# Performance work log

Hardware: AMD Instinct MI355X
Metric: run time of the kernel (lower is better)

## Reference

```python
import jax, jax.numpy as jnp
import numpy as np

LMAX = 3
D_IN = 16    # sum(2l+1) for l=0..3
D_OUT = 156  # sum over the 34 CG instructions of (2*l3+1)


def _build_sparse_cg():
    """Build the concatenated sparse CG index lists (mu1, mu2, mu3) and
    coefficients, mirroring TensorProduct.__init__: loop over all
    (l1, l2, l3) paths with l3 <= LMAX, take nonzeros of the real-basis
    Wigner-3j tensor (nonzero pattern: |m1' +- m2'| == |m3'|), offset the
    indices by the per-irrep block offsets, and concatenate.
    Coefficient values are deterministic synthetic stand-ins with the
    correct sparsity structure and component-normalization scale."""
    rs = np.random.RandomState(0)
    off_in = [0, 1, 4, 9]  # block offsets for l = 0..3 (block dim 2l+1)
    mu1, mu2, mu3, vals = [], [], [], []
    off3 = 0
    for l1 in range(LMAX + 1):
        for l2 in range(LMAX + 1):
            for l3 in range(abs(l1 - l2), min(l1 + l2, LMAX) + 1):
                for m1 in range(2 * l1 + 1):
                    for m2 in range(2 * l2 + 1):
                        a, b = m1 - l1, m2 - l2
                        for m3 in range(2 * l3 + 1):
                            c = m3 - l3
                            if abs(a + b) == abs(c) or abs(a - b) == abs(c):
                                mu1.append(off_in[l1] + m1)
                                mu2.append(off_in[l2] + m2)
                                mu3.append(off3 + m3)
                                vals.append(rs.randn() / np.sqrt(2 * l3 + 1))
                off3 += 2 * l3 + 1
    assert off3 == D_OUT
    return (np.asarray(mu1, np.int32), np.asarray(mu2, np.int32),
            np.asarray(mu3, np.int32), np.asarray(vals, np.float32))


def setup_inputs() -> dict:
    key = jax.random.key(0)
    k1, k2 = jax.random.split(key)
    B, C = 1024, 128
    x = jax.random.normal(k1, (B, D_IN, C), dtype=jnp.float32)
    y = jax.random.normal(k2, (B, D_IN, C), dtype=jnp.float32)
    mu1, mu2, mu3, cg = _build_sparse_cg()
    return {
        "x": x,
        "y": y,
        "cg": jnp.asarray(cg),
        "mu1": jnp.asarray(mu1),
        "mu2": jnp.asarray(mu2),
        "mu3": jnp.asarray(mu3),
    }


def reference(x, y, cg, mu1, mu2, mu3):
    # Fused equivalent of the per-batch / per-instruction Python loops:
    # out[b, mu3[k], c] += cg[k] * x[b, mu1[k], c] * y[b, mu2[k], c]
    terms = x[:, mu1, :] * cg[None, :, None] * y[:, mu2, :]  # [B, K, C]
    out = jnp.zeros((x.shape[0], D_OUT, x.shape[2]), dtype=x.dtype)
    return out.at[:, mu3, :].add(terms)
```

## Files before the change

### kernel.cpp

```cpp
#include <hip/hip_runtime.h>
#include <utility>


#define D_IN_ 16
#define D_OUT_ 156
#define C_ 128
#define KMAX_ 2048

struct CGRows {
    int n;
    int start[D_OUT_ + 1];
    int k[KMAX_];
    int m1[KMAX_];
    int m2[KMAX_];
};

constexpr CGRows build_rows() {
    int mu1[KMAX_] = {}, mu2[KMAX_] = {}, mu3[KMAX_] = {};
    int n = 0;
    const int off_in[4] = {0, 1, 4, 9};
    int off3 = 0;
    for (int l1 = 0; l1 <= 3; ++l1) {
        for (int l2 = 0; l2 <= 3; ++l2) {
            int lo = l1 > l2 ? l1 - l2 : l2 - l1;
            int hi = (l1 + l2) < 3 ? (l1 + l2) : 3;
            for (int l3 = lo; l3 <= hi; ++l3) {
                for (int m1 = 0; m1 < 2 * l1 + 1; ++m1) {
                    for (int m2 = 0; m2 < 2 * l2 + 1; ++m2) {
                        int a = m1 - l1, b = m2 - l2;
                        for (int m3 = 0; m3 < 2 * l3 + 1; ++m3) {
                            int c = m3 - l3;
                            int s = a + b; if (s < 0) s = -s;
                            int d = a - b; if (d < 0) d = -d;
                            int e = c < 0 ? -c : c;
                            if (s == e || d == e) {
                                mu1[n] = off_in[l1] + m1;
                                mu2[n] = off_in[l2] + m2;
                                mu3[n] = off3 + m3;
                                ++n;
                            }
                        }
                    }
                }
                off3 += 2 * l3 + 1;
            }
        }
    }
    CGRows r{};
    r.n = n;
    int cnt[D_OUT_] = {};
    for (int i = 0; i < n; ++i) cnt[mu3[i]]++;
    r.start[0] = 0;
    for (int j = 0; j < D_OUT_; ++j) r.start[j + 1] = r.start[j] + cnt[j];
    int pos[D_OUT_] = {};
    for (int j = 0; j < D_OUT_; ++j) pos[j] = r.start[j];
    for (int i = 0; i < n; ++i) {
        int j = mu3[i];
        int p = pos[j]++;
        r.k[p] = i;
        r.m1[p] = mu1[i];
        r.m2[p] = mu2[i];
    }
    return r;
}

constexpr CGRows CG = build_rows();
constexpr int K = CG.n;
static_assert(K <= KMAX_, "KMAX too small");

constexpr int find_split() {
    int j = 0;
    while (CG.start[j] < CG.n / 2) ++j;
    return j;
}
constexpr int RSPLIT = find_split();

constexpr unsigned need1(int j0, int j1) {
    unsigned m = 0;
    for (int p = CG.start[j0]; p < CG.start[j1]; ++p) m |= 1u << CG.m1[p];
    return m;
}
constexpr unsigned need2(int j0, int j1) {
    unsigned m = 0;
    for (int p = CG.start[j0]; p < CG.start[j1]; ++p) m |= 1u << CG.m2[p];
    return m;
}

__device__ __constant__ CGRows dCG = build_rows();

__global__ void gather_cg(const float* __restrict__ cg, float* __restrict__ cgs) {
    int i = blockIdx.x * 256 + threadIdx.x;
    if (i < K) cgs[i] = cg[dCG.k[i]];
}

template <unsigned M, int I>
__device__ __forceinline__ void load1(float2 (&v)[D_IN_], const float* __restrict__ base) {
    if constexpr ((M >> I) & 1u) v[I] = *(const float2*)(base + I * C_);
    else v[I] = make_float2(0.0f, 0.0f);
}

template <unsigned M, int... Is>
__device__ __forceinline__ void load_masked(float2 (&v)[D_IN_], const float* __restrict__ base,
                                            std::integer_sequence<int, Is...>) {
    (load1<M, Is>(v, base), ...);
}

template <int Base, int... Ts>
__device__ __forceinline__ float2 row_sum2(const float* __restrict__ cgs,
                                           const float2 (&xv)[D_IN_],
                                           const float2 (&yv)[D_IN_],
                                           std::integer_sequence<int, Ts...>) {
    float2 s = make_float2(0.0f, 0.0f);
    (((s.x = fmaf(cgs[Base + Ts], xv[CG.m1[Base + Ts]].x * yv[CG.m2[Base + Ts]].x, s.x)),
      (s.y = fmaf(cgs[Base + Ts], xv[CG.m1[Base + Ts]].y * yv[CG.m2[Base + Ts]].y, s.y))), ...);
    return s;
}

template <int J>
__device__ __forceinline__ void store_row(float* __restrict__ ob, const float* __restrict__ cgs,
                                          const float2 (&xv)[D_IN_], const float2 (&yv)[D_IN_]) {
    constexpr int base = CG.start[J];
    constexpr int nt = CG.start[J + 1] - CG.start[J];
    float2 s = row_sum2<base>(cgs, xv, yv, std::make_integer_sequence<int, nt>{});
    *(float2*)(ob + J * C_) = s;
}

template <int J0, int... Js>
__device__ __forceinline__ void rows_range(float* __restrict__ ob, const float* __restrict__ cgs,
                                           const float2 (&xv)[D_IN_], const float2 (&yv)[D_IN_],
                                           std::integer_sequence<int, Js...>) {
    (store_row<J0 + Js>(ob, cgs, xv, yv), ...);
}

__global__ __launch_bounds__(256, 2) void tp_cg_kernel(
    const float* __restrict__ x, const float* __restrict__ y,
    const float* __restrict__ cgs, float* __restrict__ out) {
    const int tid = (int)threadIdx.x;
    const int c2 = tid & 63;
    const int half = (tid >> 6) & 1;
    const int b = (int)((blockIdx.x << 1) | (tid >> 7));

    const float* xb = x + (size_t)b * (D_IN_ * C_) + c2 * 2;
    const float* yb = y + (size_t)b * (D_IN_ * C_) + c2 * 2;
    float* ob = out + (size_t)b * (D_OUT_ * C_) + c2 * 2;

    float2 xv[D_IN_], yv[D_IN_];
    if (half == 0) {
        constexpr unsigned m1 = need1(0, RSPLIT), m2 = need2(0, RSPLIT);
        load_masked<m1>(xv, xb, std::make_integer_sequence<int, D_IN_>{});
        load_masked<m2>(yv, yb, std::make_integer_sequence<int, D_IN_>{});
        rows_range<0>(ob, cgs, xv, yv, std::make_integer_sequence<int, RSPLIT>{});
    } else {
        constexpr unsigned m1 = need1(RSPLIT, D_OUT_), m2 = need2(RSPLIT, D_OUT_);
        load_masked<m1>(xv, xb, std::make_integer_sequence<int, D_IN_>{});
        load_masked<m2>(yv, yb, std::make_integer_sequence<int, D_IN_>{});
        rows_range<RSPLIT>(ob, cgs, xv, yv, std::make_integer_sequence<int, D_OUT_ - RSPLIT>{});
    }
}

extern "C" void kernel_launch(void* const* d_in, const int* in_sizes, int n_in,
                              void* d_out, int out_size, void* d_ws, size_t ws_size,
                              hipStream_t stream) {
    const float* x  = (const float*)d_in[0];
    const float* y  = (const float*)d_in[1];
    const float* cg = (const float*)d_in[2];
    float* out = (float*)d_out;
    float* cgs = (float*)d_ws;

    const int B = in_sizes[0] / (D_IN_ * C_);

    gather_cg<<<(K + 255) / 256, 256, 0, stream>>>(cg, cgs);

    const int nblocks = B / 2;
    tp_cg_kernel<<<nblocks, 256, 0, stream>>>(x, y, cgs, out);
}
```

Measured before the change: 109.5 us.

## Split output rows into quarters with one channel per thread

Work is now split four ways over the output rows instead of two, and each thread handles a single channel with scalar loads and stores instead of float2. The grid grows to four times as many blocks, and launch bounds are raised to ask for four blocks per SIMD-occupancy unit. The aim is more parallelism and less register pressure per thread, which should improve latency hiding. In exchange, input rows shared between quarters are loaded more than once, and the narrower 4-byte accesses give up the wider vector memory transactions.

```diff
diff --git a/kernel.cpp b/kernel.cpp
--- a/kernel.cpp
+++ b/kernel.cpp
@@ -68,12 +68,13 @@
 constexpr int K = CG.n;
 static_assert(K <= KMAX_, "KMAX too small");
 
-constexpr int find_split() {
+constexpr int findq(int i) {
+    int target = (CG.n * i) / 4;
     int j = 0;
-    while (CG.start[j] < CG.n / 2) ++j;
+    while (CG.start[j] < target) ++j;
     return j;
 }
-constexpr int RSPLIT = find_split();
+constexpr int QS0 = 0, QS1 = findq(1), QS2 = findq(2), QS3 = findq(3), QS4 = D_OUT_;
 
 constexpr unsigned need1(int j0, int j1) {
     unsigned m = 0;
@@ -94,68 +95,70 @@
 }
 
 template <unsigned M, int I>
-__device__ __forceinline__ void load1(float2 (&v)[D_IN_], const float* __restrict__ base) {
-    if constexpr ((M >> I) & 1u) v[I] = *(const float2*)(base + I * C_);
-    else v[I] = make_float2(0.0f, 0.0f);
+__device__ __forceinline__ void load1(float (&v)[D_IN_], const float* __restrict__ base) {
+    if constexpr ((M >> I) & 1u) v[I] = base[I * C_];
+    else v[I] = 0.0f;
 }
 
 template <unsigned M, int... Is>
-__device__ __forceinline__ void load_masked(float2 (&v)[D_IN_], const float* __restrict__ base,
+__device__ __forceinline__ void load_masked(float (&v)[D_IN_], const float* __restrict__ base,
                                             std::integer_sequence<int, Is...>) {
     (load1<M, Is>(v, base), ...);
 }
 
 template <int Base, int... Ts>
-__device__ __forceinline__ float2 row_sum2(const float* __restrict__ cgs,
-                                           const float2 (&xv)[D_IN_],
-                                           const float2 (&yv)[D_IN_],
-                                           std::integer_sequence<int, Ts...>) {
-    float2 s = make_float2(0.0f, 0.0f);
-    (((s.x = fmaf(cgs[Base + Ts], xv[CG.m1[Base + Ts]].x * yv[CG.m2[Base + Ts]].x, s.x)),
-      (s.y = fmaf(cgs[Base + Ts], xv[CG.m1[Base + Ts]].y * yv[CG.m2[Base + Ts]].y, s.y))), ...);
+__device__ __forceinline__ float row_sum(const float* __restrict__ cgs,
+                                         const float (&xv)[D_IN_],
+                                         const float (&yv)[D_IN_],
+                                         std::integer_sequence<int, Ts...>) {
+    float s = 0.0f;
+    ((s = fmaf(cgs[Base + Ts], xv[CG.m1[Base + Ts]] * yv[CG.m2[Base + Ts]], s)), ...);
     return s;
 }
 
 template <int J>
 __device__ __forceinline__ void store_row(float* __restrict__ ob, const float* __restrict__ cgs,
-                                          const float2 (&xv)[D_IN_], const float2 (&yv)[D_IN_]) {
+                                          const float (&xv)[D_IN_], const float (&yv)[D_IN_]) {
     constexpr int base = CG.start[J];
     constexpr int nt = CG.start[J + 1] - CG.start[J];
-    float2 s = row_sum2<base>(cgs, xv, yv, std::make_integer_sequence<int, nt>{});
-    *(float2*)(ob + J * C_) = s;
+    ob[J * C_] = row_sum<base>(cgs, xv, yv, std::make_integer_sequence<int, nt>{});
 }
 
 template <int J0, int... Js>
 __device__ __forceinline__ void rows_range(float* __restrict__ ob, const float* __restrict__ cgs,
-                                           const float2 (&xv)[D_IN_], const float2 (&yv)[D_IN_],
+                                           const float (&xv)[D_IN_], const float (&yv)[D_IN_],
                                            std::integer_sequence<int, Js...>) {
     (store_row<J0 + Js>(ob, cgs, xv, yv), ...);
 }
 
-__global__ __launch_bounds__(256, 2) void tp_cg_kernel(
+template <int J0, int J1>
+__device__ __forceinline__ void do_range(const float* __restrict__ xb,
+                                         const float* __restrict__ yb,
+                                         float* __restrict__ ob,
+                                         const float* __restrict__ cgs) {
+    constexpr unsigned M1 = need1(J0, J1), M2 = need2(J0, J1);
+    float xv[D_IN_], yv[D_IN_];
+    load_masked<M1>(xv, xb, std::make_integer_sequence<int, D_IN_>{});
+    load_masked<M2>(yv, yb, std::make_integer_sequence<int, D_IN_>{});
+    rows_range<J0>(ob, cgs, xv, yv, std::make_integer_sequence<int, J1 - J0>{});
+}
+
+__global__ __launch_bounds__(256, 4) void tp_cg_kernel(
     const float* __restrict__ x, const float* __restrict__ y,
     const float* __restrict__ cgs, float* __restrict__ out) {
     const int tid = (int)threadIdx.x;
-    const int c2 = tid & 63;
-    const int half = (tid >> 6) & 1;
-    const int b = (int)((blockIdx.x << 1) | (tid >> 7));
+    const int c = tid & (C_ - 1);
+    const int b = (int)(blockIdx.x >> 1);
+    const int q = (int)(((blockIdx.x & 1) << 1) | (tid >> 7));
 
-    const float* xb = x + (size_t)b * (D_IN_ * C_) + c2 * 2;
-    const float* yb = y + (size_t)b * (D_IN_ * C_) + c2 * 2;
-    float* ob = out + (size_t)b * (D_OUT_ * C_) + c2 * 2;
+    const float* xb = x + (size_t)b * (D_IN_ * C_) + c;
+    const float* yb = y + (size_t)b * (D_IN_ * C_) + c;
+    float* ob = out + (size_t)b * (D_OUT_ * C_) + c;
 
-    float2 xv[D_IN_], yv[D_IN_];
-    if (half == 0) {
-        constexpr unsigned m1 = need1(0, RSPLIT), m2 = need2(0, RSPLIT);
-        load_masked<m1>(xv, xb, std::make_integer_sequence<int, D_IN_>{});
-        load_masked<m2>(yv, yb, std::make_integer_sequence<int, D_IN_>{});
-        rows_range<0>(ob, cgs, xv, yv, std::make_integer_sequence<int, RSPLIT>{});
-    } else {
-        constexpr unsigned m1 = need1(RSPLIT, D_OUT_), m2 = need2(RSPLIT, D_OUT_);
-        load_masked<m1>(xv, xb, std::make_integer_sequence<int, D_IN_>{});
-        load_masked<m2>(yv, yb, std::make_integer_sequence<int, D_IN_>{});
-        rows_range<RSPLIT>(ob, cgs, xv, yv, std::make_integer_sequence<int, D_OUT_ - RSPLIT>{});
-    }
+    if (q == 0)      do_range<QS0, QS1>(xb, yb, ob, cgs);
+    else if (q == 1) do_range<QS1, QS2>(xb, yb, ob, cgs);
+    else if (q == 2) do_range<QS2, QS3>(xb, yb, ob, cgs);
+    else             do_range<QS3, QS4>(xb, yb, ob, cgs);
 }
 
 extern "C" void kernel_launch(void* const* d_in, const int* in_sizes, int n_in,
@@ -171,6 +174,5 @@
 
     gather_cg<<<(K + 255) / 256, 256, 0, stream>>>(cg, cgs);
 
-    const int nblocks = B / 2;
-    tp_cg_kernel<<<nblocks, 256, 0, stream>>>(x, y, cgs, out);
+    tp_cg_kernel<<<B * 2, 256, 0, stream>>>(x, y, cgs, out);
 }
```

New measurement: 112.5 us. 2.7% more time.
